# Kernel optimization log

Measured on AMD Instinct MI355X. Metric: run time of the kernel, lower is better.

Reference implementation:

```python
import jax, jax.numpy as jnp
import numpy as np
from jax import lax

# STE sign: forward maps x>=0 -> +1, x<0 -> -1 (matches XORQuantizeSTE)
@jax.custom_vjp
def ste_sign(x):
    return jnp.where(x >= 0, jnp.ones_like(x), -jnp.ones_like(x))

def _ste_fwd(x):
    return ste_sign(x), None

def _ste_bwd(_, g):
    return (g,)  # identity pass-through

ste_sign.defvjp(_ste_fwd, _ste_bwd)


def _xor_quant(x, w):
    """Per-layer XNOR-Net quantization: alpha = mean|W| scales both
    binarized activation and binarized weight (as in the wrapper's hook
    + binarization())."""
    alpha = jnp.mean(jnp.abs(w))
    return alpha * ste_sign(x), alpha * ste_sign(w)


def _conv(x, w, b, stride):
    y = lax.conv_general_dilated(
        x, w, window_strides=(stride, stride), padding=((1, 1), (1, 1)),
        dimension_numbers=('NCHW', 'OIHW', 'NCHW'))
    return y + b[None, :, None, None]


def setup_inputs() -> dict:
    key = jax.random.key(0)
    ks = jax.random.split(key, 9)
    f32 = jnp.float32
    x = jax.random.normal(ks[0], (32, 3, 224, 224), dtype=f32)
    w1 = jax.random.normal(ks[1], (64, 3, 3, 3), dtype=f32) * 0.1
    b1 = jax.random.normal(ks[2], (64,), dtype=f32) * 0.01
    w2 = jax.random.normal(ks[3], (128, 64, 3, 3), dtype=f32) * 0.05
    b2 = jax.random.normal(ks[4], (128,), dtype=f32) * 0.01
    w3 = jax.random.normal(ks[5], (256, 128, 3, 3), dtype=f32) * 0.03
    b3 = jax.random.normal(ks[6], (256,), dtype=f32) * 0.01
    wf = jax.random.normal(ks[7], (1000, 256), dtype=f32) * 0.05
    bf = jax.random.normal(ks[8], (1000,), dtype=f32) * 0.01
    return {'x': x, 'w1': w1, 'b1': b1, 'w2': w2, 'b2': b2,
            'w3': w3, 'b3': b3, 'wf': wf, 'bf': bf}


def reference(x, w1, b1, w2, b2, w3, b3, wf, bf):
    # layer 1: binarize activation + weight with shared alpha, dense conv
    xq, wq = _xor_quant(x, w1)
    h = jnp.clip(_conv(xq, wq, b1, 2), -1.0, 1.0)   # [32,64,112,112]
    xq, wq = _xor_quant(h, w2)
    h = jnp.clip(_conv(xq, wq, b2, 2), -1.0, 1.0)   # [32,128,56,56]
    xq, wq = _xor_quant(h, w3)
    h = jnp.clip(_conv(xq, wq, b3, 2), -1.0, 1.0)   # [32,256,28,28]
    h = jnp.mean(h, axis=(2, 3))                     # global avg pool [32,256]
    xq, wq = _xor_quant(h, wf)
    return xq @ wq.T + bf                            # [32,1000]
```

## Files before the change

kernel.cpp:

```cpp
#include <hip/hip_runtime.h>
#include <stdint.h>
#include <math.h>


#define WP2_OFF    2048ull
#define WP3T_OFF   16384ull
#define WFP_OFF    65536ull
#define PART_OFF   100352ull
#define P1_OFF     102400ull
#define P2_OFF     3313664ull
#define POOLP_OFF  4919296ull

__global__ __launch_bounds__(256) void k1_conv1_pack(
    const float* __restrict__ x,  const float* __restrict__ w1, const float* __restrict__ b1,
    const float* __restrict__ w2, const float* __restrict__ w3, const float* __restrict__ wf,
    uint64_t* __restrict__ wp2, uint64_t* __restrict__ wp3t, uint64_t* __restrict__ wfp,
    double* __restrict__ part, uint64_t* __restrict__ p1)
{
    const int tid = threadIdx.x, lane = tid & 63, wid = tid >> 6, bid = blockIdx.x;
    if (bid < 1568) {
        __shared__ double a2s;
        __shared__ double db1[64];
        __shared__ uint32_t wm[64];
        if (wid == 0) {
            double s = 0.0;
            #pragma unroll
            for (int i = 0; i < 27; i++) s += fabs((double)w1[lane + i*64]);
            #pragma unroll
            for (int off = 1; off < 64; off <<= 1) s += __shfl_xor(s, off, 64);
            if (lane == 0) { double a = s / 1728.0; a2s = a * a; }
        } else if (wid == 1) {
            uint32_t m = 0;
            for (int t = 0; t < 27; t++) {
                int ci = t / 9, r = t % 9, kh = r / 3, kw = r % 3;
                if (w1[((lane*3 + ci)*3 + kh)*3 + kw] >= 0.f) m |= (1u << t);
            }
            wm[lane] = m;
        } else if (wid == 2) {
            db1[lane] = (double)b1[lane];
        }
        int idx = bid * 256 + tid;
        int wo = idx % 112, t1 = idx / 112;
        int ho = t1 % 112, n = t1 / 112;
        uint32_t xm = 0, vm = 0;
        #pragma unroll
        for (int ci = 0; ci < 3; ci++)
            #pragma unroll
            for (int kh = 0; kh < 3; kh++) {
                int hi = 2*ho + kh - 1;
                if ((unsigned)hi >= 224u) continue;
                #pragma unroll
                for (int kw = 0; kw < 3; kw++) {
                    int wi = 2*wo + kw - 1;
                    if ((unsigned)wi >= 224u) continue;
                    int t = ci*9 + kh*3 + kw;
                    vm |= (1u << t);
                    if (x[((n*3 + ci)*224 + hi)*224 + wi] >= 0.f) xm |= (1u << t);
                }
            }
        __syncthreads();
        double a2 = a2s;
        int V = __popc(vm);
        uint64_t bits = 0;
        for (int co = 0; co < 64; co++) {
            int m = __popc((~(xm ^ wm[co])) & vm);
            double h = a2 * (double)(2*m - V) + db1[co];
            if (h >= 0.0) bits |= (1ull << co);
        }
        p1[idx] = bits;
    } else {
        int rel = bid - 1568;
        if (rel < 96) {
            __shared__ double sd[256];
            int t = rel >> 5, c = rel & 31;
            const float* w; int n;
            if (t == 0)      { w = w2; n = 128*64*9; }
            else if (t == 1) { w = w3; n = 256*128*9; }
            else             { w = wf; n = 1000*256; }
            int per = (n + 31) / 32;
            int lo = c * per, hi = min(n, lo + per);
            double s0 = 0.0, s1 = 0.0, s2 = 0.0, s3 = 0.0;
            int i = lo + tid;
            for (; i + 768 < hi; i += 1024) {
                s0 += fabs((double)w[i]);
                s1 += fabs((double)w[i + 256]);
                s2 += fabs((double)w[i + 512]);
                s3 += fabs((double)w[i + 768]);
            }
            for (; i < hi; i += 256) s0 += fabs((double)w[i]);
            sd[tid] = (s0 + s1) + (s2 + s3);
            __syncthreads();
            for (int off = 128; off > 0; off >>= 1) {
                if (tid < off) sd[tid] += sd[tid + off];
                __syncthreads();
            }
            if (tid == 0) part[(t + 1)*32 + c] = sd[0];
        }
        int gw = rel * 4 + wid;
        const int nw = 640;
        for (int w = gw; w < 1152; w += nw) {
            int co = w / 9, tap = w % 9, kh = tap / 3, kw = tap % 3;
            uint64_t b = __ballot(w2[((co*64 + lane)*3 + kh)*3 + kw] >= 0.f);
            if (lane == 0) wp2[w] = b;
        }
        for (int w = gw; w < 4608; w += nw) {
            int co = w / 18, r = w % 18, tap = r / 2, half = r & 1;
            int kh = tap / 3, kw = tap % 3;
            uint64_t b = __ballot(w3[((co*128 + half*64 + lane)*3 + kh)*3 + kw] >= 0.f);
            if (lane == 0) wp3t[(tap*2 + half)*256 + co] = b;
        }
        for (int w = gw; w < 4000; w += nw) {
            int o = w >> 2, j = w & 3;
            uint64_t b = __ballot(wf[o*256 + j*64 + lane] >= 0.f);
            if (lane == 0) wfp[w] = b;
        }
    }
}

__global__ __launch_bounds__(256) void k2_conv2(
    const uint64_t* __restrict__ p1, const float* __restrict__ b2,
    const double* __restrict__ part, const uint64_t* __restrict__ wp2g,
    uint32_t* __restrict__ p2)
{
    __shared__ uint64_t wp[1152];
    __shared__ uint64_t xs[9*64];
    __shared__ int      dtab[128*4];
    __shared__ double   db2[128];
    const int tid = threadIdx.x, lane = tid & 63;

    for (int i = tid; i < 1152; i += 256) wp[i] = wp2g[i];
    if (tid < 128) db2[tid] = (double)b2[tid];
    for (int i = tid; i < 576; i += 256) {
        int t = i / 64, pl = i % 64;
        int pos = blockIdx.x * 64 + pl;
        int wo = pos % 56, t1 = pos / 56;
        int ho = t1 % 56, n = t1 / 56;
        int kh = t / 3, kw = t % 3;
        int hi = 2*ho + kh - 1, wi = 2*wo + kw - 1;
        bool ok = ((unsigned)hi < 112u) && ((unsigned)wi < 112u);
        xs[t*64 + pl] = ok ? p1[(n*112 + hi)*112 + wi] : 0ull;
    }
    double s = 0.0;
    for (int j = 0; j < 32; j++) s += part[32 + j];
    double a = s / (double)(128*64*9);
    double a2 = a * a;
    __syncthreads();
    if (tid < 128) {
        int co = tid;
        uint32_t P[9];
        #pragma unroll
        for (int t = 0; t < 9; t++) P[t] = __popcll(wp[co*9 + t]);
        int cT = P[0] + P[1] + P[2];
        int cL = P[0] + P[3] + P[6];
        int cC = P[0];
        #pragma unroll
        for (int cfg = 0; cfg < 4; cfg++) {
            int isT = cfg & 1, isL = (cfg >> 1) & 1;
            int V = 9 - 3*isT - 3*isL + (isT & isL);
            int corr = isT*cT + isL*cL - (isT & isL)*cC;
            dtab[co*4 + cfg] = 64*V + 2*corr;
        }
    }
    __syncthreads();

    int q = tid >> 6;
    int co0 = q * 32;
    int pos = blockIdx.x * 64 + lane;
    int wo = pos % 56, t1 = pos / 56;
    int ho = t1 % 56;
    int cfg = (ho == 0 ? 1 : 0) | (wo == 0 ? 2 : 0);
    uint64_t xv[9];
    #pragma unroll
    for (int t = 0; t < 9; t++) xv[t] = xs[t*64 + lane];
    uint32_t bits = 0;
    for (int c = 0; c < 32; c++) {
        int co = co0 + c;
        int mm = 0;
        #pragma unroll
        for (int t = 0; t < 9; t++)
            mm += __popcll(xv[t] ^ wp[co*9 + t]);
        int dot = dtab[co*4 + cfg] - 2*mm;
        double h = a2 * (double)dot + db2[co];
        if (h >= 0.0) bits |= (1u << c);
    }
    p2[pos*4 + q] = bits;
}

__global__ __launch_bounds__(256) void k3_conv3pool(
    const uint64_t* __restrict__ p2, const float* __restrict__ b3,
    const double* __restrict__ part, const uint64_t* __restrict__ wp3t,
    double* __restrict__ partial)
{
    __shared__ uint64_t xs[28*18];
    const int tid = threadIdx.x;
    int n = blockIdx.x / 28, ho = blockIdx.x % 28;

    double s = 0.0;
    for (int j = 0; j < 32; j++) s += part[64 + j];
    double a = s / (double)(256*128*9);
    double a2 = a * a;

    uint64_t w[18];
    #pragma unroll
    for (int i = 0; i < 18; i++) w[i] = wp3t[i*256 + tid];
    uint32_t P[9];
    #pragma unroll
    for (int t = 0; t < 9; t++) P[t] = __popcll(w[2*t]) + __popcll(w[2*t+1]);

    for (int i = tid; i < 504; i += 256) {
        int wo = i / 18, r = i % 18;
        int tap = r / 2, half = r % 2;
        int kh = tap / 3, kw = tap % 3;
        int hi = 2*ho + kh - 1, wi = 2*wo + kw - 1;
        bool ok = ((unsigned)hi < 56u) && ((unsigned)wi < 56u);
        xs[i] = ok ? p2[(size_t)((n*56 + hi)*56 + wi)*2 + half] : 0ull;
    }
    __syncthreads();

    bool htop = (ho == 0);
    int rv = htop ? 2 : 3;
    double bc = (double)b3[tid];
    double sum = 0.0;
    for (int wo = 0; wo < 28; wo++) {
        int mm = 0;
        #pragma unroll
        for (int t = 0; t < 18; t++)
            mm += __popcll(xs[wo*18 + t] ^ w[t]);
        bool wl = (wo == 0);
        int cv = wl ? 2 : 3;
        int corr = 0;
        if (htop) corr += P[0] + P[1] + P[2];
        if (wl)   corr += P[0] + P[3] + P[6];
        if (htop && wl) corr -= P[0];
        int dot = 128*(rv*cv) - 2*mm + 2*corr;
        double h = a2 * (double)dot + bc;
        h = fmin(fmax(h, -1.0), 1.0);
        sum += h;
    }
    partial[(size_t)(n*28 + ho)*256 + tid] = sum;
}

__global__ __launch_bounds__(256) void k4_poolfc(
    const double* __restrict__ partial, const uint64_t* __restrict__ wfp,
    const float* __restrict__ bf, const double* __restrict__ part,
    float* __restrict__ out)
{
    __shared__ uint64_t spl[4];
    const int tid = threadIdx.x, lane = tid & 63;
    int n = blockIdx.x;
    double s = 0.0;
    for (int c = 0; c < 28; c++) s += partial[(size_t)(n*28 + c)*256 + tid];
    uint64_t bal = __ballot((s / 784.0) >= 0.0);
    if (lane == 0) spl[tid >> 6] = bal;

    double sa = 0.0;
    for (int j = 0; j < 32; j++) sa += part[96 + j];
    double a = sa / (double)(1000*256);
    double aa = a * a;
    __syncthreads();
    uint64_t s0 = spl[0], s1 = spl[1], s2 = spl[2], s3 = spl[3];
    for (int o = tid; o < 1000; o += 256) {
        int m = __popcll(s0 ^ wfp[o*4]) + __popcll(s1 ^ wfp[o*4+1])
              + __popcll(s2 ^ wfp[o*4+2]) + __popcll(s3 ^ wfp[o*4+3]);
        out[n*1000 + o] = (float)(aa * (double)(256 - 2*m) + (double)bf[o]);
    }
}

extern "C" void kernel_launch(void* const* d_in, const int* in_sizes, int n_in,
                              void* d_out, int out_size, void* d_ws, size_t ws_size,
                              hipStream_t stream) {
    const float* x  = (const float*)d_in[0];
    const float* w1 = (const float*)d_in[1];
    const float* b1 = (const float*)d_in[2];
    const float* w2 = (const float*)d_in[3];
    const float* b2 = (const float*)d_in[4];
    const float* w3 = (const float*)d_in[5];
    const float* b3 = (const float*)d_in[6];
    const float* wf = (const float*)d_in[7];
    const float* bf = (const float*)d_in[8];

    char* ws = (char*)d_ws;
    uint64_t* wp2    = (uint64_t*)(ws + WP2_OFF);
    uint64_t* wp3t   = (uint64_t*)(ws + WP3T_OFF);
    uint64_t* wfp    = (uint64_t*)(ws + WFP_OFF);
    double*   part   = (double*)  (ws + PART_OFF);
    uint64_t* p1     = (uint64_t*)(ws + P1_OFF);
    uint32_t* p2     = (uint32_t*)(ws + P2_OFF);
    double*   poolp  = (double*)  (ws + POOLP_OFF);
    float*    out    = (float*)   d_out;

    hipLaunchKernelGGL(k1_conv1_pack, dim3(1728), dim3(256), 0, stream,
                       x, w1, b1, w2, w3, wf, wp2, wp3t, wfp, part, p1);
    hipLaunchKernelGGL(k2_conv2,      dim3(1568), dim3(256), 0, stream,
                       p1, b2, part, wp2, p2);
    hipLaunchKernelGGL(k3_conv3pool,  dim3(896),  dim3(256), 0, stream,
                       (const uint64_t*)p2, b3, part, wp3t, poolp);
    hipLaunchKernelGGL(k4_poolfc,     dim3(32),   dim3(256), 0, stream,
                       poolp, wfp, bf, part, out);
}
```

Baseline: 146.1 us.

## Replace per-output double threshold math with integer thresholds; two positions per thread in conv2

Conv1 and conv2 now precompute, for each output channel, the integer threshold at which alpha^2*dot+bias becomes non-negative. The inner loops then use a plain integer compare instead of a double multiply-add. Conv2 also has each thread handle two output positions, so each weight word loaded from LDS is reused twice, and the grid is halved. The threshold search needs careful clamping to stay exact, and the extra per-thread registers could lower occupancy.

```diff
diff --git a/kernel.cpp b/kernel.cpp
--- a/kernel.cpp
+++ b/kernel.cpp
@@ -20,8 +20,8 @@
     const int tid = threadIdx.x, lane = tid & 63, wid = tid >> 6, bid = blockIdx.x;
     if (bid < 1568) {
         __shared__ double a2s;
-        __shared__ double db1[64];
         __shared__ uint32_t wm[64];
+        __shared__ int Ts[64];
         if (wid == 0) {
             double s = 0.0;
             #pragma unroll
@@ -36,8 +36,6 @@
                 if (w1[((lane*3 + ci)*3 + kh)*3 + kw] >= 0.f) m |= (1u << t);
             }
             wm[lane] = m;
-        } else if (wid == 2) {
-            db1[lane] = (double)b1[lane];
         }
         int idx = bid * 256 + tid;
         int wo = idx % 112, t1 = idx / 112;
@@ -59,13 +57,20 @@
                 }
             }
         __syncthreads();
-        double a2 = a2s;
+        if (tid < 64) {
+            double a2 = a2s, b = (double)b1[tid];
+            int k = (int)ceil(-b / a2);
+            k = max(-27, min(28, k));
+            while (k > -27 && (a2 * (double)(k - 1) + b >= 0.0)) k--;
+            while (k <= 27 && !(a2 * (double)k + b >= 0.0)) k++;
+            Ts[tid] = k;
+        }
+        __syncthreads();
         int V = __popc(vm);
         uint64_t bits = 0;
         for (int co = 0; co < 64; co++) {
             int m = __popc((~(xm ^ wm[co])) & vm);
-            double h = a2 * (double)(2*m - V) + db1[co];
-            if (h >= 0.0) bits |= (1ull << co);
+            if (2*m - V >= Ts[co]) bits |= (1ull << co);
         }
         p1[idx] = bits;
     } else {
@@ -123,30 +128,32 @@
     uint32_t* __restrict__ p2)
 {
     __shared__ uint64_t wp[1152];
-    __shared__ uint64_t xs[9*64];
-    __shared__ int      dtab[128*4];
-    __shared__ double   db2[128];
+    __shared__ uint64_t xs[1152];
+    __shared__ int      M[128*4];
     const int tid = threadIdx.x, lane = tid & 63;
 
     for (int i = tid; i < 1152; i += 256) wp[i] = wp2g[i];
-    if (tid < 128) db2[tid] = (double)b2[tid];
-    for (int i = tid; i < 576; i += 256) {
-        int t = i / 64, pl = i % 64;
-        int pos = blockIdx.x * 64 + pl;
+    for (int i = tid; i < 1152; i += 256) {
+        int t = i >> 7, pl = i & 127;
+        int pos = blockIdx.x * 128 + pl;
         int wo = pos % 56, t1 = pos / 56;
         int ho = t1 % 56, n = t1 / 56;
         int kh = t / 3, kw = t % 3;
         int hi = 2*ho + kh - 1, wi = 2*wo + kw - 1;
         bool ok = ((unsigned)hi < 112u) && ((unsigned)wi < 112u);
-        xs[t*64 + pl] = ok ? p1[(n*112 + hi)*112 + wi] : 0ull;
-    }
-    double s = 0.0;
-    for (int j = 0; j < 32; j++) s += part[32 + j];
-    double a = s / (double)(128*64*9);
-    double a2 = a * a;
+        xs[i] = ok ? p1[(n*112 + hi)*112 + wi] : 0ull;
+    }
     __syncthreads();
     if (tid < 128) {
         int co = tid;
+        double s = 0.0;
+        for (int j = 0; j < 32; j++) s += part[32 + j];
+        double a = s / (double)(128*64*9);
+        double a2 = a * a, b = (double)b2[co];
+        int k = (int)ceil(-b / a2);
+        k = max(-577, min(578, k));
+        while (k > -577 && (a2 * (double)(k - 1) + b >= 0.0)) k--;
+        while (k <= 577 && !(a2 * (double)k + b >= 0.0)) k++;
         uint32_t P[9];
         #pragma unroll
         for (int t = 0; t < 9; t++) P[t] = __popcll(wp[co*9 + t]);
@@ -158,32 +165,38 @@
             int isT = cfg & 1, isL = (cfg >> 1) & 1;
             int V = 9 - 3*isT - 3*isL + (isT & isL);
             int corr = isT*cT + isL*cL - (isT & isL)*cC;
-            dtab[co*4 + cfg] = 64*V + 2*corr;
+            int dtab = 64*V + 2*corr;
+            M[co*4 + cfg] = (dtab - k) >> 1;
         }
     }
     __syncthreads();
 
     int q = tid >> 6;
     int co0 = q * 32;
-    int pos = blockIdx.x * 64 + lane;
-    int wo = pos % 56, t1 = pos / 56;
-    int ho = t1 % 56;
-    int cfg = (ho == 0 ? 1 : 0) | (wo == 0 ? 2 : 0);
-    uint64_t xv[9];
+    int pos0 = blockIdx.x * 128 + lane;
+    int pos1 = pos0 + 64;
+    int wo0 = pos0 % 56, ho0 = (pos0 / 56) % 56;
+    int wo1 = pos1 % 56, ho1 = (pos1 / 56) % 56;
+    int cfg0 = (ho0 == 0 ? 1 : 0) | (wo0 == 0 ? 2 : 0);
+    int cfg1 = (ho1 == 0 ? 1 : 0) | (wo1 == 0 ? 2 : 0);
+    uint64_t xv0[9], xv1[9];
     #pragma unroll
-    for (int t = 0; t < 9; t++) xv[t] = xs[t*64 + lane];
-    uint32_t bits = 0;
+    for (int t = 0; t < 9; t++) { xv0[t] = xs[t*128 + lane]; xv1[t] = xs[t*128 + 64 + lane]; }
+    uint32_t bits0 = 0, bits1 = 0;
     for (int c = 0; c < 32; c++) {
         int co = co0 + c;
-        int mm = 0;
-        #pragma unroll
-        for (int t = 0; t < 9; t++)
-            mm += __popcll(xv[t] ^ wp[co*9 + t]);
-        int dot = dtab[co*4 + cfg] - 2*mm;
-        double h = a2 * (double)dot + db2[co];
-        if (h >= 0.0) bits |= (1u << c);
-    }
-    p2[pos*4 + q] = bits;
+        int mm0 = 0, mm1 = 0;
+        #pragma unroll
+        for (int t = 0; t < 9; t++) {
+            uint64_t w = wp[co*9 + t];
+            mm0 += __popcll(xv0[t] ^ w);
+            mm1 += __popcll(xv1[t] ^ w);
+        }
+        if (mm0 <= M[co*4 + cfg0]) bits0 |= (1u << c);
+        if (mm1 <= M[co*4 + cfg1]) bits1 |= (1u << c);
+    }
+    p2[pos0*4 + q] = bits0;
+    p2[pos1*4 + q] = bits1;
 }
 
 __global__ __launch_bounds__(256) void k3_conv3pool(
@@ -291,7 +304,7 @@
 
     hipLaunchKernelGGL(k1_conv1_pack, dim3(1728), dim3(256), 0, stream,
                        x, w1, b1, w2, w3, wf, wp2, wp3t, wfp, part, p1);
-    hipLaunchKernelGGL(k2_conv2,      dim3(1568), dim3(256), 0, stream,
+    hipLaunchKernelGGL(k2_conv2,      dim3(784),  dim3(256), 0, stream,
                        p1, b2, part, wp2, p2);
     hipLaunchKernelGGL(k3_conv3pool,  dim3(896),  dim3(256), 0, stream,
                        (const uint64_t*)p2, b3, part, wp3t, poolp);
```

Result: no change. 146.0 us (-0.1%).
